# Kernel tuning notes

Measured on AMD Instinct MI355X. Metric: run time of the kernel, lower is better.

The kernel has to match this reference:

```python
import jax, jax.numpy as jnp
import numpy as np

TOP_K = 20
BN_EPS = 1e-5

B, F, D, O = 2048, 16384, 512, 4096


def setup_inputs() -> dict:
    key = jax.random.key(0)
    ks = jax.random.split(key, 4)
    return {
        "sae_features": jax.random.uniform(ks[0], (B, F), jnp.float32),  # nonneg SAE activations
        "emb": jax.random.normal(ks[1], (F, D), jnp.float32) * (1.0 / np.sqrt(D)),
        "lin_w": jax.random.normal(ks[2], (O, F), jnp.float32) * (1.0 / np.sqrt(F)),
        "lin_b": jnp.zeros((O,), jnp.float32),
        "global_bias": jnp.zeros((O,), jnp.float32),
        "bn1_gamma": jnp.ones((D,), jnp.float32),
        "bn1_beta": jnp.zeros((D,), jnp.float32),
        "mlp_w1": jax.random.normal(ks[3], (D, D), jnp.float32) * np.sqrt(2.0 / D),
        "mlp_b1": jnp.zeros((D,), jnp.float32),
        "bn2_gamma": jnp.ones((D,), jnp.float32),
        "bn2_beta": jnp.zeros((D,), jnp.float32),
        "mlp_w2": jax.random.normal(jax.random.fold_in(key, 7), (O, D), jnp.float32) * np.sqrt(2.0 / D),
        "mlp_b2": jnp.zeros((O,), jnp.float32),
    }


def _batchnorm(x, gamma, beta):
    # training-mode BatchNorm1d: biased batch statistics, eps=1e-5
    mean = jnp.mean(x, axis=0)
    var = jnp.var(x, axis=0)
    return (x - mean) * jax.lax.rsqrt(var + BN_EPS) * gamma + beta


def reference(sae_features, emb, lin_w, lin_b, global_bias, bn1_gamma, bn1_beta,
              mlp_w1, mlp_b1, bn2_gamma, bn2_beta, mlp_w2, mlp_b2):
    b = sae_features.shape[0]
    # --- top-k sparsification (keep top 20 activations per row, zero the rest) ---
    top_vals, top_idx = jax.lax.top_k(sae_features, TOP_K)  # [B, K]
    x = jnp.zeros_like(sae_features).at[jnp.arange(b)[:, None], top_idx].set(top_vals)
    # --- bi-interaction pooling: 0.5*((x@E)^2 - (x^2)@(E^2)) ---
    # algebraically identical to the broadcast multiply-sum in the source
    sum_emb = x @ emb                      # [B, D]
    sum_sq = (x * x) @ (emb * emb)          # [B, D]
    bi = 0.5 * (sum_emb * sum_emb - sum_sq)
    # --- BN + interaction MLP (dropout = identity in eval) ---
    h = _batchnorm(bi, bn1_gamma, bn1_beta)
    h = h @ mlp_w1.T + mlp_b1
    h = jax.nn.relu(_batchnorm(h, bn2_gamma, bn2_beta))
    interaction_out = h @ mlp_w2.T + mlp_b2  # [B, O]
    # --- linear component on the ORIGINAL (non-sparsified) features ---
    linear_out = sae_features @ lin_w.T + lin_b  # [B, O]
    output = global_bias[None, :] + linear_out + interaction_out
    return output, linear_out, interaction_out
```

## Files before the change

### kernel.cpp

```cpp
#include <hip/hip_runtime.h>

#define B_ 2048
#define F_ 16384
#define D_ 512
#define O_ 4096

typedef __attribute__((ext_vector_type(8))) short bf16x8;
typedef __attribute__((ext_vector_type(4))) float f32x4;
typedef unsigned long long ull;

__device__ inline unsigned short f2bf(float f) {
    unsigned u = __float_as_uint(f);
    u += 0x7FFFu + ((u >> 16) & 1u);
    return (unsigned short)(u >> 16);
}

__device__ inline void glds16(const void* g, void* l) {
    __builtin_amdgcn_global_load_lds((const __attribute__((address_space(1))) void*)g,
                                     (__attribute__((address_space(3))) void*)l, 16, 0, 0);
}

__global__ void cvt_bf16_kernel(const float* __restrict__ s, unsigned short* __restrict__ d, int n4) {
    int stride = gridDim.x * blockDim.x;
    for (int i = blockIdx.x * blockDim.x + threadIdx.x; i < n4; i += stride) {
        float4 v = ((const float4*)s)[i];
        ushort4 o;
        o.x = f2bf(v.x); o.y = f2bf(v.y); o.z = f2bf(v.z); o.w = f2bf(v.w);
        ((ushort4*)d)[i] = o;
    }
}

__global__ __launch_bounds__(256) void topk1_kernel(const float* __restrict__ sae,
        ull* __restrict__ cand, unsigned short* __restrict__ sae_bf) {
    __shared__ ull maxk[256];
    __shared__ ull cbuf[160];
    int tid = threadIdx.x;
    int chunk = blockIdx.x, row = blockIdx.y;
    size_t rbase = (size_t)row * F_ + chunk * 2048;
    const float4* src4 = (const float4*)(sae + rbase);
    ushort4* dst4 = (ushort4*)(sae_bf + rbase);

    float4 va = src4[tid], vb = src4[tid + 256];
    ushort4 oa, ob;
    oa.x = f2bf(va.x); oa.y = f2bf(va.y); oa.z = f2bf(va.z); oa.w = f2bf(va.w);
    ob.x = f2bf(vb.x); ob.y = f2bf(vb.y); ob.z = f2bf(vb.z); ob.w = f2bf(vb.w);
    dst4[tid] = oa; dst4[tid + 256] = ob;

    int c0 = chunk * 2048 + 4 * tid;
#define MKKEY(v, c) ((((ull)__float_as_uint(v)) << 32) | (unsigned)(~(c)))
    ull k0 = MKKEY(va.x, c0 + 0), k1 = MKKEY(va.y, c0 + 1);
    ull k2 = MKKEY(va.z, c0 + 2), k3 = MKKEY(va.w, c0 + 3);
    ull k4 = MKKEY(vb.x, c0 + 1024), k5 = MKKEY(vb.y, c0 + 1025);
    ull k6 = MKKEY(vb.z, c0 + 1026), k7 = MKKEY(vb.w, c0 + 1027);
#undef MKKEY
#define CE(a, b) { ull x_ = a, y_ = b; ull h_ = x_ > y_ ? x_ : y_; ull l_ = x_ > y_ ? y_ : x_; a = h_; b = l_; }
    CE(k0,k1) CE(k2,k3) CE(k4,k5) CE(k6,k7)
    CE(k0,k2) CE(k1,k3) CE(k4,k6) CE(k5,k7)
    CE(k1,k2) CE(k5,k6)
    CE(k0,k4) CE(k1,k5) CE(k2,k6) CE(k3,k7)
    CE(k2,k4) CE(k3,k5)
    CE(k1,k2) CE(k3,k4) CE(k5,k6)
#undef CE

    maxk[tid] = k0;
    __syncthreads();
    int r = 0;
    for (int k = 0; k < 256; ++k) r += (maxk[k] > k0);
    if (r < 20) {
        ull* o = cbuf + r * 8;
        o[0]=k0; o[1]=k1; o[2]=k2; o[3]=k3; o[4]=k4; o[5]=k5; o[6]=k6; o[7]=k7;
    }
    __syncthreads();
    ull myc = (tid < 160) ? cbuf[tid] : 0ull;
    int r2 = 0;
    for (int k = 0; k < 160; ++k) r2 += (cbuf[k] > myc);
    if (tid < 160 && r2 < 20)
        cand[((size_t)row * 8 + chunk) * 20 + r2] = myc;
}

__global__ __launch_bounds__(256) void bi_kernel(const ull* __restrict__ cand,
        const float* __restrict__ emb, float* __restrict__ bi) {
    __shared__ ull c[160];
    __shared__ int   si[20];
    __shared__ float sv[20];
    int tid = threadIdx.x, row = blockIdx.x;
    if (tid < 160) c[tid] = cand[(size_t)row * 160 + tid];
    __syncthreads();
    if (tid < 160) {
        ull m = c[tid];
        int r = 0;
        for (int k = 0; k < 160; ++k) r += (c[k] > m);
        if (r < 20) {
            sv[r] = __uint_as_float((unsigned)(m >> 32));
            si[r] = (int)(~(unsigned)m);
        }
    }
    __syncthreads();
    float s0 = 0.f, q0 = 0.f, s1 = 0.f, q1 = 0.f;
    int d0 = tid, d1 = tid + 256;
#pragma unroll
    for (int k = 0; k < 20; ++k) {
        float v = sv[k];
        const float* e = emb + (size_t)si[k] * D_;
        float e0 = e[d0], e1 = e[d1];
        s0 += v * e0; q0 += v * v * e0 * e0;
        s1 += v * e1; q1 += v * v * e1 * e1;
    }
    bi[(size_t)row * D_ + d0] = 0.5f * (s0 * s0 - q0);
    bi[(size_t)row * D_ + d1] = 0.5f * (s1 * s1 - q1);
}

__global__ __launch_bounds__(256) void colpart_kernel(const float* __restrict__ X,
        float* __restrict__ ps, float* __restrict__ pq, int N) {
    __shared__ float4 ls[128], lq[128];
    int tid = threadIdx.x;
    int c4 = tid & 127, half = tid >> 7;
    int r0 = blockIdx.x * 32 + half;
    float4 s = {0.f, 0.f, 0.f, 0.f}, q = {0.f, 0.f, 0.f, 0.f};
#pragma unroll
    for (int i = 0; i < 16; ++i) {
        float4 x = ((const float4*)(X + (size_t)(r0 + 2 * i) * N))[c4];
        s.x += x.x; s.y += x.y; s.z += x.z; s.w += x.w;
        q.x += x.x * x.x; q.y += x.y * x.y; q.z += x.z * x.z; q.w += x.w * x.w;
    }
    if (half) { ls[c4] = s; lq[c4] = q; }
    __syncthreads();
    if (!half) {
        float4 s2 = ls[c4], q2 = lq[c4];
        s.x += s2.x; s.y += s2.y; s.z += s2.z; s.w += s2.w;
        q.x += q2.x; q.y += q2.y; q.z += q2.z; q.w += q2.w;
        ((float4*)(ps + (size_t)blockIdx.x * N))[c4] = s;
        ((float4*)(pq + (size_t)blockIdx.x * N))[c4] = q;
    }
}

__global__ __launch_bounds__(256) void colfin_kernel(const float* __restrict__ ps,
        const float* __restrict__ pq, const float* __restrict__ gamma,
        const float* __restrict__ beta, float* __restrict__ scale,
        float* __restrict__ shift, int npart, int N, int M) {
    int col = blockIdx.x * 256 + threadIdx.x;
    if (col >= N) return;
    float s = 0.f, q = 0.f;
    for (int k = 0; k < npart; ++k) {
        s += ps[(size_t)k * N + col];
        q += pq[(size_t)k * N + col];
    }
    float mean = s / M;
    float var = q / M - mean * mean;
    float sc = gamma[col] * rsqrtf(var + 1e-5f);
    scale[col] = sc;
    shift[col] = beta[col] - mean * sc;
}

__global__ void bn_apply_kernel(const float* __restrict__ X, const float* __restrict__ scale,
        const float* __restrict__ shift, unsigned short* __restrict__ Y,
        int n4, int colmask4, int relu) {
    int stride = gridDim.x * blockDim.x;
    for (int i = blockIdx.x * blockDim.x + threadIdx.x; i < n4; i += stride) {
        float4 x = ((const float4*)X)[i];
        int c = (i & colmask4) * 4;
        float4 sc = *(const float4*)(scale + c);
        float4 sh = *(const float4*)(shift + c);
        float y0 = x.x * sc.x + sh.x;
        float y1 = x.y * sc.y + sh.y;
        float y2 = x.z * sc.z + sh.z;
        float y3 = x.w * sc.w + sh.w;
        if (relu) {
            y0 = fmaxf(y0, 0.f); y1 = fmaxf(y1, 0.f);
            y2 = fmaxf(y2, 0.f); y3 = fmaxf(y3, 0.f);
        }
        ushort4 o;
        o.x = f2bf(y0); o.y = f2bf(y1); o.z = f2bf(y2); o.w = f2bf(y3);
        ((ushort4*)Y)[i] = o;
    }
}

template <bool FUSE>
__global__ __launch_bounds__(512) void gemm8w_kernel(const unsigned short* __restrict__ A,
        const unsigned short* __restrict__ W, const float* __restrict__ bias,
        float* __restrict__ out, const float* __restrict__ lin,
        const float* __restrict__ gb, float* __restrict__ out0,
        int M, int N, int K) {
    __shared__ short As[3 * 4096];
    __shared__ short Bs[3 * 4096];
    int tid = threadIdx.x;
    int lane = tid & 63, w = tid >> 6;
    int wr = w >> 2, wc = w & 3;
    int l15 = lane & 15, lhi = lane >> 4;
    int xk = (l15 >> 1) & 3;
    int rchunk = (lhi ^ xk) << 3;

    int nwg = gridDim.x * gridDim.y;
    int bid = blockIdx.y * gridDim.x + blockIdx.x;
    int s = (bid & 7) * (nwg >> 3) + (bid >> 3);
    int gsz = gridDim.x << 3;
    int g = s / gsz, r = s % gsz;
    int by = (g << 3) + (r & 7);
    int bx = r >> 3;
    int bm = by * 128, bn = bx * 128;

    int rA = tid >> 2;
    int kp = tid & 3;
    int kps = kp ^ ((rA >> 1) & 3);
    const unsigned short* gA = A + (size_t)(bm + rA) * K + kps * 8;
    const unsigned short* gB = W + (size_t)(bn + rA) * K + kps * 8;

    f32x4 acc[4][2];
#pragma unroll
    for (int i = 0; i < 4; ++i)
#pragma unroll
        for (int j = 0; j < 2; ++j) { f32x4 z = {0.f, 0.f, 0.f, 0.f}; acc[i][j] = z; }

    auto STAGE = [&](int t, int buf) {
        int k0 = t << 5;
        glds16(gA + k0, (char*)(As + buf * 4096) + w * 1024);
        glds16(gB + k0, (char*)(Bs + buf * 4096) + w * 1024);
    };
    auto LOADF = [&](bf16x8* af, bf16x8* bv, int buf) {
        const short* Ab = As + buf * 4096;
        const short* Bb = Bs + buf * 4096;
#pragma unroll
        for (int mi = 0; mi < 4; ++mi)
            af[mi] = *(const bf16x8*)&Ab[(wr * 64 + mi * 16 + l15) * 32 + rchunk];
#pragma unroll
        for (int ni = 0; ni < 2; ++ni)
            bv[ni] = *(const bf16x8*)&Bb[(wc * 32 + ni * 16 + l15) * 32 + rchunk];
    };
    auto MFMA8 = [&](const bf16x8* af, const bf16x8* bv) {
#pragma unroll
        for (int mi = 0; mi < 4; ++mi)
#pragma unroll
            for (int ni = 0; ni < 2; ++ni)
                acc[mi][ni] = __builtin_amdgcn_mfma_f32_16x16x32_bf16(af[mi], bv[ni], acc[mi][ni], 0, 0, 0);
    };

    int NT = K >> 5;

    STAGE(0, 0);
    STAGE(1, 1);
    asm volatile("s_waitcnt vmcnt(2)" ::: "memory");
    __builtin_amdgcn_sched_barrier(0);
    __builtin_amdgcn_s_barrier();
    __builtin_amdgcn_sched_barrier(0);

    bf16x8 afA[4], bvA[2], afB[4], bvB[2];
    LOADF(afA, bvA, 0);

    for (int t = 0; t + 4 <= NT; t += 2) {
        STAGE(t + 2, (t + 2) % 3);
        asm volatile("s_waitcnt lgkmcnt(0)" ::: "memory");
        __builtin_amdgcn_sched_barrier(0);
        asm volatile("s_waitcnt vmcnt(2)" ::: "memory");
        __builtin_amdgcn_sched_barrier(0);
        __builtin_amdgcn_s_barrier();
        __builtin_amdgcn_sched_barrier(0);
        LOADF(afB, bvB, (t + 1) % 3);
        __builtin_amdgcn_s_setprio(1);
        MFMA8(afA, bvA);
        __builtin_amdgcn_s_setprio(0);
        __builtin_amdgcn_sched_group_barrier(0x100, 6, 0);
        __builtin_amdgcn_sched_group_barrier(0x008, 8, 0);
        STAGE(t + 3, (t + 3) % 3);
        asm volatile("s_waitcnt lgkmcnt(0)" ::: "memory");
        __builtin_amdgcn_sched_barrier(0);
        asm volatile("s_waitcnt vmcnt(2)" ::: "memory");
        __builtin_amdgcn_sched_barrier(0);
        __builtin_amdgcn_s_barrier();
        __builtin_amdgcn_sched_barrier(0);
        LOADF(afA, bvA, (t + 2) % 3);
        __builtin_amdgcn_s_setprio(1);
        MFMA8(afB, bvB);
        __builtin_amdgcn_s_setprio(0);
        __builtin_amdgcn_sched_group_barrier(0x100, 6, 0);
        __builtin_amdgcn_sched_group_barrier(0x008, 8, 0);
    }
    asm volatile("s_waitcnt lgkmcnt(0)" ::: "memory");
    __builtin_amdgcn_sched_barrier(0);
    asm volatile("s_waitcnt vmcnt(0)" ::: "memory");
    __builtin_amdgcn_sched_barrier(0);
    __builtin_amdgcn_s_barrier();
    __builtin_amdgcn_sched_barrier(0);
    LOADF(afB, bvB, (NT - 1) % 3);
    __builtin_amdgcn_s_setprio(1);
    MFMA8(afA, bvA);
    __builtin_amdgcn_s_setprio(0);
    asm volatile("s_waitcnt lgkmcnt(0)" ::: "memory");
    __builtin_amdgcn_sched_barrier(0);
    __builtin_amdgcn_s_setprio(1);
    MFMA8(afB, bvB);
    __builtin_amdgcn_s_setprio(0);

#pragma unroll
    for (int mi = 0; mi < 4; ++mi)
#pragma unroll
        for (int ni = 0; ni < 2; ++ni) {
            int col = bn + wc * 32 + ni * 16 + l15;
            float bb = bias[col];
            float gbv = FUSE ? gb[col] : 0.f;
            int row0 = bm + wr * 64 + mi * 16 + lhi * 4;
#pragma unroll
            for (int r2 = 0; r2 < 4; ++r2) {
                size_t idx = (size_t)(row0 + r2) * N + col;
                float v = acc[mi][ni][r2] + bb;
                out[idx] = v;
                if (FUSE) out0[idx] = gbv + lin[idx] + v;
            }
        }
}

extern "C" void kernel_launch(void* const* d_in, const int* in_sizes, int n_in,
                              void* d_out, int out_size, void* d_ws, size_t ws_size,
                              hipStream_t stream) {
    const float* sae  = (const float*)d_in[0];
    const float* emb  = (const float*)d_in[1];
    const float* lin_w = (const float*)d_in[2];
    const float* lin_b = (const float*)d_in[3];
    const float* gbias = (const float*)d_in[4];
    const float* bn1g = (const float*)d_in[5];
    const float* bn1b = (const float*)d_in[6];
    const float* w1   = (const float*)d_in[7];
    const float* b1   = (const float*)d_in[8];
    const float* bn2g = (const float*)d_in[9];
    const float* bn2b = (const float*)d_in[10];
    const float* w2   = (const float*)d_in[11];
    const float* b2   = (const float*)d_in[12];
    float* out = (float*)d_out;
    const size_t BO = (size_t)B_ * O_;

    char* ws = (char*)d_ws;
    auto alloc = [&](size_t bytes) -> char* {
        char* p = ws;
        ws += (bytes + 255) & ~(size_t)255;
        return p;
    };
    unsigned short* sae_bf  = (unsigned short*)alloc((size_t)B_ * F_ * 2);
    unsigned short* linw_bf = (unsigned short*)alloc((size_t)O_ * F_ * 2);
    unsigned short* w1_bf   = (unsigned short*)alloc((size_t)D_ * D_ * 2);
    unsigned short* w2_bf   = (unsigned short*)alloc((size_t)O_ * D_ * 2);
    unsigned short* a1_bf   = (unsigned short*)alloc((size_t)B_ * D_ * 2);
    unsigned short* h2_bf   = (unsigned short*)alloc((size_t)B_ * D_ * 2);
    ull*   cand = (ull*)alloc((size_t)B_ * 160 * 8);
    float* bi = (float*)alloc((size_t)B_ * D_ * 4);
    float* h1 = (float*)alloc((size_t)B_ * D_ * 4);
    float* ps = (float*)alloc(64 * D_ * 4);
    float* pq = (float*)alloc(64 * D_ * 4);
    float* sc1 = (float*)alloc(D_ * 4);
    float* sh1 = (float*)alloc(D_ * 4);
    float* sc2 = (float*)alloc(D_ * 4);
    float* sh2 = (float*)alloc(D_ * 4);

    cvt_bf16_kernel<<<2048, 256, 0, stream>>>(lin_w, linw_bf, (int)((size_t)O_ * F_ / 4));
    cvt_bf16_kernel<<<256, 256, 0, stream>>>(w1, w1_bf, D_ * D_ / 4);
    cvt_bf16_kernel<<<1024, 256, 0, stream>>>(w2, w2_bf, O_ * D_ / 4);

    topk1_kernel<<<dim3(8, B_), 256, 0, stream>>>(sae, cand, sae_bf);

    bi_kernel<<<B_, 256, 0, stream>>>(cand, emb, bi);

    colpart_kernel<<<64, 256, 0, stream>>>(bi, ps, pq, D_);
    colfin_kernel<<<2, 256, 0, stream>>>(ps, pq, bn1g, bn1b, sc1, sh1, 64, D_, B_);
    bn_apply_kernel<<<1024, 256, 0, stream>>>(bi, sc1, sh1, a1_bf, B_ * D_ / 4, D_ / 4 - 1, 0);
    gemm8w_kernel<false><<<dim3(D_ / 128, B_ / 128), 512, 0, stream>>>(
        a1_bf, w1_bf, b1, h1, nullptr, nullptr, nullptr, B_, D_, D_);

    colpart_kernel<<<64, 256, 0, stream>>>(h1, ps, pq, D_);
    colfin_kernel<<<2, 256, 0, stream>>>(ps, pq, bn2g, bn2b, sc2, sh2, 64, D_, B_);
    bn_apply_kernel<<<1024, 256, 0, stream>>>(h1, sc2, sh2, h2_bf, B_ * D_ / 4, D_ / 4 - 1, 1);

    gemm8w_kernel<false><<<dim3(O_ / 128, B_ / 128), 512, 0, stream>>>(
        sae_bf, linw_bf, lin_b, out + BO, nullptr, nullptr, nullptr, B_, O_, F_);

    gemm8w_kernel<true><<<dim3(O_ / 128, B_ / 128), 512, 0, stream>>>(
        h2_bf, w2_bf, b2, out + 2 * BO, out + BO, gbias, out, B_, O_, D_);
}
```

Measured before the change: 620.2 us.

## Add 256x128 triple-buffered bf16 GEMM kernel for the large linear layer

```diff
diff --git a/kernel.cpp b/kernel.cpp
--- a/kernel.cpp
+++ b/kernel.cpp
@@ -308,6 +308,154 @@
         }
 }
 
+__global__ __launch_bounds__(512) void gemm256_kernel(const unsigned short* __restrict__ A,
+        const unsigned short* __restrict__ W, const float* __restrict__ bias,
+        float* __restrict__ out, int M, int N, int K) {
+    __shared__ short As[3 * 16384];
+    __shared__ short Bs[3 * 8192];
+    int tid = threadIdx.x;
+    int l = tid & 63, w = tid >> 6;
+    int wm = w >> 1, wn = w & 1;
+    int l15 = l & 15, lhi = l >> 4;
+    int lr = l >> 3, lc = l & 7;
+    int sc = lc ^ lr;
+
+    int bid = blockIdx.y * gridDim.x + blockIdx.x;
+    int s = (bid & 7) * ((gridDim.x * gridDim.y) >> 3) + (bid >> 3);
+    int by = s & 7, bx = s >> 3;
+    int bm = by * 256, bn = bx * 128;
+
+    const unsigned short* gA0 = A + (size_t)(bm +   0 + w * 8 + lr) * K + sc * 8;
+    const unsigned short* gA1 = A + (size_t)(bm +  64 + w * 8 + lr) * K + sc * 8;
+    const unsigned short* gA2 = A + (size_t)(bm + 128 + w * 8 + lr) * K + sc * 8;
+    const unsigned short* gA3 = A + (size_t)(bm + 192 + w * 8 + lr) * K + sc * 8;
+    const unsigned short* gB0 = W + (size_t)(bn +   0 + w * 8 + lr) * K + sc * 8;
+    const unsigned short* gB1 = W + (size_t)(bn +  64 + w * 8 + lr) * K + sc * 8;
+
+    int xk7 = l15 & 7;
+    int aR0 = (wm * 64 +  0 + l15) << 7;
+    int aR1 = (wm * 64 + 16 + l15) << 7;
+    int aR2 = (wm * 64 + 32 + l15) << 7;
+    int aR3 = (wm * 64 + 48 + l15) << 7;
+    int bR0 = (wn * 64 +  0 + l15) << 7;
+    int bR1 = (wn * 64 + 16 + l15) << 7;
+    int bR2 = (wn * 64 + 32 + l15) << 7;
+    int bR3 = (wn * 64 + 48 + l15) << 7;
+    int c0 = ((0 + lhi) ^ xk7) << 4;
+    int c1 = ((4 + lhi) ^ xk7) << 4;
+
+    f32x4 acc[4][4];
+#pragma unroll
+    for (int i = 0; i < 4; ++i)
+#pragma unroll
+        for (int j = 0; j < 4; ++j) { f32x4 z = {0.f, 0.f, 0.f, 0.f}; acc[i][j] = z; }
+
+    const char* AsB = (const char*)As;
+    const char* BsB = (const char*)Bs;
+#define RDA(rr, cc, bo) (*(const bf16x8*)(AsB + (bo) + (rr) + (cc)))
+#define RDB(rr, cc, bo) (*(const bf16x8*)(BsB + (bo) + (rr) + (cc)))
+
+    bf16x8 a0, a1, a2, a3, b0, b1, b2, b3;
+#define MFMA_N01() { \
+    acc[0][0] = __builtin_amdgcn_mfma_f32_16x16x32_bf16(a0, b0, acc[0][0], 0, 0, 0); \
+    acc[0][1] = __builtin_amdgcn_mfma_f32_16x16x32_bf16(a0, b1, acc[0][1], 0, 0, 0); \
+    acc[1][0] = __builtin_amdgcn_mfma_f32_16x16x32_bf16(a1, b0, acc[1][0], 0, 0, 0); \
+    acc[1][1] = __builtin_amdgcn_mfma_f32_16x16x32_bf16(a1, b1, acc[1][1], 0, 0, 0); \
+    acc[2][0] = __builtin_amdgcn_mfma_f32_16x16x32_bf16(a2, b0, acc[2][0], 0, 0, 0); \
+    acc[2][1] = __builtin_amdgcn_mfma_f32_16x16x32_bf16(a2, b1, acc[2][1], 0, 0, 0); \
+    acc[3][0] = __builtin_amdgcn_mfma_f32_16x16x32_bf16(a3, b0, acc[3][0], 0, 0, 0); \
+    acc[3][1] = __builtin_amdgcn_mfma_f32_16x16x32_bf16(a3, b1, acc[3][1], 0, 0, 0); }
+#define MFMA_N23() { \
+    acc[0][2] = __builtin_amdgcn_mfma_f32_16x16x32_bf16(a0, b2, acc[0][2], 0, 0, 0); \
+    acc[0][3] = __builtin_amdgcn_mfma_f32_16x16x32_bf16(a0, b3, acc[0][3], 0, 0, 0); \
+    acc[1][2] = __builtin_amdgcn_mfma_f32_16x16x32_bf16(a1, b2, acc[1][2], 0, 0, 0); \
+    acc[1][3] = __builtin_amdgcn_mfma_f32_16x16x32_bf16(a1, b3, acc[1][3], 0, 0, 0); \
+    acc[2][2] = __builtin_amdgcn_mfma_f32_16x16x32_bf16(a2, b2, acc[2][2], 0, 0, 0); \
+    acc[2][3] = __builtin_amdgcn_mfma_f32_16x16x32_bf16(a2, b3, acc[2][3], 0, 0, 0); \
+    acc[3][2] = __builtin_amdgcn_mfma_f32_16x16x32_bf16(a3, b2, acc[3][2], 0, 0, 0); \
+    acc[3][3] = __builtin_amdgcn_mfma_f32_16x16x32_bf16(a3, b3, acc[3][3], 0, 0, 0); }
+#define LGKM0  { asm volatile("s_waitcnt lgkmcnt(0)" ::: "memory"); __builtin_amdgcn_sched_barrier(0); }
+#define BAR    { __builtin_amdgcn_s_barrier(); __builtin_amdgcn_sched_barrier(0); }
+
+    int NT = K >> 6;
+
+    {
+        int dA = w * 1024, dB = w * 1024;
+        glds16(gA0, (char*)As + dA);           glds16(gA1, (char*)As + 8192 + dA);
+        glds16(gA2, (char*)As + 16384 + dA);   glds16(gA3, (char*)As + 24576 + dA);
+        glds16(gB0, (char*)Bs + dB);           glds16(gB1, (char*)Bs + 8192 + dB);
+        glds16(gA0 + 64, (char*)As + 32768 + dA);         glds16(gA1 + 64, (char*)As + 32768 + 8192 + dA);
+        glds16(gA2 + 64, (char*)As + 32768 + 16384 + dA); glds16(gA3 + 64, (char*)As + 32768 + 24576 + dA);
+        glds16(gB0 + 64, (char*)Bs + 16384 + dB);         glds16(gB1 + 64, (char*)Bs + 16384 + 8192 + dB);
+    }
+    asm volatile("s_waitcnt vmcnt(6)" ::: "memory");
+    __builtin_amdgcn_sched_barrier(0);
+    BAR;
+
+    int cur = 0;
+    for (int t = 0; t < NT; ++t) {
+        int s2 = cur + 2; if (s2 >= 3) s2 -= 3;
+        int Abo = cur * 32768, Bbo = cur * 16384;
+        int AboS = s2 * 32768, BboS = s2 * 16384;
+        int kst = (t + 2) << 6;
+        bool st = (t + 2) < NT;
+        int dA = w * 1024;
+
+        a0 = RDA(aR0, c0, Abo); a1 = RDA(aR1, c0, Abo);
+        a2 = RDA(aR2, c0, Abo); a3 = RDA(aR3, c0, Abo);
+        b0 = RDB(bR0, c0, Bbo); b1 = RDB(bR1, c0, Bbo);
+        if (st) { glds16(gA0 + kst, (char*)As + AboS + dA);
+                  glds16(gA1 + kst, (char*)As + AboS + 8192 + dA); }
+        BAR; LGKM0;
+        __builtin_amdgcn_s_setprio(1); MFMA_N01(); __builtin_amdgcn_s_setprio(0);
+        BAR;
+        b2 = RDB(bR2, c0, Bbo); b3 = RDB(bR3, c0, Bbo);
+        if (st) { glds16(gA2 + kst, (char*)As + AboS + 16384 + dA);
+                  glds16(gA3 + kst, (char*)As + AboS + 24576 + dA); }
+        BAR; LGKM0;
+        __builtin_amdgcn_s_setprio(1); MFMA_N23(); __builtin_amdgcn_s_setprio(0);
+        BAR;
+        a0 = RDA(aR0, c1, Abo); a1 = RDA(aR1, c1, Abo);
+        a2 = RDA(aR2, c1, Abo); a3 = RDA(aR3, c1, Abo);
+        b0 = RDB(bR0, c1, Bbo); b1 = RDB(bR1, c1, Bbo);
+        if (st) { glds16(gB0 + kst, (char*)Bs + BboS + dA); }
+        BAR; LGKM0;
+        __builtin_amdgcn_s_setprio(1); MFMA_N01(); __builtin_amdgcn_s_setprio(0);
+        BAR;
+        b2 = RDB(bR2, c1, Bbo); b3 = RDB(bR3, c1, Bbo);
+        if (st) { glds16(gB1 + kst, (char*)Bs + BboS + 8192 + dA); }
+        BAR; LGKM0;
+        __builtin_amdgcn_s_setprio(1); MFMA_N23(); __builtin_amdgcn_s_setprio(0);
+        if (t + 1 < NT) {
+            if (t + 2 < NT) { asm volatile("s_waitcnt vmcnt(6)" ::: "memory"); }
+            else            { asm volatile("s_waitcnt vmcnt(0)" ::: "memory"); }
+            __builtin_amdgcn_sched_barrier(0);
+            BAR;
+        }
+        ++cur; if (cur >= 3) cur = 0;
+    }
+#undef RDA
+#undef RDB
+#undef MFMA_N01
+#undef MFMA_N23
+#undef LGKM0
+#undef BAR
+
+#pragma unroll
+    for (int mi = 0; mi < 4; ++mi)
+#pragma unroll
+        for (int ni = 0; ni < 4; ++ni) {
+            int col = bn + wn * 64 + ni * 16 + l15;
+            float bb = bias[col];
+            int row0 = bm + wm * 64 + mi * 16 + lhi * 4;
+#pragma unroll
+            for (int r2 = 0; r2 < 4; ++r2) {
+                size_t idx = (size_t)(row0 + r2) * N + col;
+                out[idx] = acc[mi][ni][r2] + bb;
+            }
+        }
+}
+
 extern "C" void kernel_launch(void* const* d_in, const int* in_sizes, int n_in,
                               void* d_out, int out_size, void* d_ws, size_t ws_size,
                               hipStream_t stream) {
@@ -367,8 +515,8 @@
     colfin_kernel<<<2, 256, 0, stream>>>(ps, pq, bn2g, bn2b, sc2, sh2, 64, D_, B_);
     bn_apply_kernel<<<1024, 256, 0, stream>>>(h1, sc2, sh2, h2_bf, B_ * D_ / 4, D_ / 4 - 1, 1);
 
-    gemm8w_kernel<false><<<dim3(O_ / 128, B_ / 128), 512, 0, stream>>>(
-        sae_bf, linw_bf, lin_b, out + BO, nullptr, nullptr, nullptr, B_, O_, F_);
+    gemm256_kernel<<<dim3(O_ / 128, B_ / 256), 512, 0, stream>>>(
+        sae_bf, linw_bf, lin_b, out + BO, B_, O_, F_);
 
     gemm8w_kernel<true><<<dim3(O_ / 128, B_ / 128), 512, 0, stream>>>(
         h2_bf, w2_bf, b2, out + 2 * BO, out + BO, gbias, out, B_, O_, D_);
```

After: 731.1 us. 1.18x slower.
